# Optimization experiments

Measured on AMD Instinct MI355X. Metric: run time of the kernel, lower is better.

Reference implementation:

```python
import jax, jax.numpy as jnp
import numpy as np

L, H, D, DH, FF, CTX, S, V = 12, 12, 768, 64, 3072, 1536, 8, 1024
B, T = 2, 1024


def setup_inputs() -> dict:
    key = jax.random.key(0)
    ks = jax.random.split(key, 12)
    init = lambda k, shape, fan_in: jax.random.normal(k, shape, jnp.float32) * (fan_in ** -0.5)
    return {
        "prev_tokens": jax.random.randint(ks[0], (B, T, S), 0, V),
        "positions": jnp.tile(jnp.arange(T, dtype=jnp.int32), (B, 1)),
        "intent_vec": jax.random.normal(ks[1], (B, 1, D), jnp.float32) * 0.02,
        "rvq_embed": jax.random.normal(ks[2], (S, V, D), jnp.float32) * 0.02,
        "pos_embed": jax.random.normal(ks[3], (CTX, D), jnp.float32) * 0.02,
        "norm1_w": jnp.ones((L, D), jnp.float32),
        "norm2_w": jnp.ones((L, D), jnp.float32),
        "qkv_w": init(ks[4], (L, 3 * D, D), D),
        "proj_w": init(ks[5], (L, D, D), D),
        "gate_w": init(ks[6], (L, FF, D), D),
        "up_w": init(ks[7], (L, FF, D), D),
        "down_w": init(ks[8], (L, D, FF), FF),
        "normf_w": jnp.ones((D,), jnp.float32),
        "heads_w": init(ks[9], (S, V, D), D),
    }


def _rmsnorm(x, w, eps=1e-6):
    return x * jax.lax.rsqrt(jnp.mean(x * x, axis=-1, keepdims=True) + eps) * w


def reference(prev_tokens, positions, intent_vec, rvq_embed, pos_embed,
              norm1_w, norm2_w, qkv_w, proj_w, gate_w, up_w, down_w,
              normf_w, heads_w):
    # 8-way RVQ embedding sum + positional + intent  -> [B, T, D]
    stage_idx = jnp.arange(S)[None, None, :]               # [1,1,S]
    x = rvq_embed[stage_idx, prev_tokens].sum(axis=2)      # gather [B,T,S,D] -> sum
    x = x + pos_embed[positions] + intent_vec

    scale = DH ** -0.5
    mask = jnp.tril(jnp.ones((T, T), dtype=bool))          # causal (prefill path)

    for l in range(L):
        # attention block (pre-norm)
        h = _rmsnorm(x, norm1_w[l])
        qkv = jnp.einsum('btd,ed->bte', h, qkv_w[l]).reshape(B, T, 3, H, DH)
        q = jnp.moveaxis(qkv[:, :, 0], 1, 2)               # [B,H,T,DH]
        k = jnp.moveaxis(qkv[:, :, 1], 1, 2)
        v = jnp.moveaxis(qkv[:, :, 2], 1, 2)
        att = jnp.einsum('bhqd,bhkd->bhqk', q, k) * scale
        att = jnp.where(mask, att, -jnp.inf)
        att = jax.nn.softmax(att, axis=-1)
        o = jnp.einsum('bhqk,bhkd->bhqd', att, v)
        o = jnp.moveaxis(o, 1, 2).reshape(B, T, D)
        x = x + jnp.einsum('btd,ed->bte', o, proj_w[l])
        # SwiGLU FFN block
        h = _rmsnorm(x, norm2_w[l])
        g = jax.nn.silu(jnp.einsum('btd,fd->btf', h, gate_w[l]))
        u = jnp.einsum('btd,fd->btf', h, up_w[l])
        x = x + jnp.einsum('btf,df->btd', g * u, down_w[l])

    x = _rmsnorm(x, normf_w)
    last = x[:, -1, :]                                     # [B, D]
    logits = jnp.einsum('bd,svd->sbv', last, heads_w)      # per-stage logits [S,B,V]
    return logits
```

## Files before the change

### kernel.cpp

```cpp
#include <hip/hip_runtime.h>
#include <hip/hip_bf16.h>

#define LAYERS 12
#define NH     12
#define D      768
#define DH     64
#define FF     3072
#define NS     8
#define NV     1024
#define BB     2
#define TT     1024
#define BT     (BB*TT)

typedef __attribute__((ext_vector_type(8))) short  short8;
typedef __attribute__((ext_vector_type(8))) unsigned short ushort8;
typedef __attribute__((ext_vector_type(4))) float  floatx4;

__device__ __forceinline__ float wave_sum(float v) {
    v += __shfl_xor(v, 1);  v += __shfl_xor(v, 2);  v += __shfl_xor(v, 4);
    v += __shfl_xor(v, 8);  v += __shfl_xor(v, 16); v += __shfl_xor(v, 32);
    return v;
}
__device__ __forceinline__ unsigned short f2bf(float f) {
    unsigned int u = __builtin_bit_cast(unsigned int, f);
    u += 0x7fffu + ((u >> 16) & 1u);
    return (unsigned short)(u >> 16);
}
__device__ __forceinline__ ushort8 pack8(float4 f0, float4 f1) {
    ushort8 r;
    r[0]=f2bf(f0.x); r[1]=f2bf(f0.y); r[2]=f2bf(f0.z); r[3]=f2bf(f0.w);
    r[4]=f2bf(f1.x); r[5]=f2bf(f1.y); r[6]=f2bf(f1.z); r[7]=f2bf(f1.w);
    return r;
}
__device__ __forceinline__ void gl2lds16(const void* g, void* l) {
    __builtin_amdgcn_global_load_lds(
        (const __attribute__((address_space(1))) unsigned int*)g,
        (__attribute__((address_space(3))) unsigned int*)l, 16, 0, 0);
}

__global__ __launch_bounds__(256) void cvt_bf16_kernel(
    const float* __restrict__ w, unsigned short* __restrict__ o, int n8) {
    const int i = blockIdx.x * 256 + threadIdx.x;
    if (i < n8) {
        const float* p = w + (size_t)i * 8;
        float4 f0 = *(const float4*)p;
        float4 f1 = *(const float4*)(p + 4);
        *(ushort8*)(o + (size_t)i * 8) = pack8(f0, f1);
    }
}

__global__ __launch_bounds__(256) void embed_kernel(
    const int* __restrict__ prev_tokens, const int* __restrict__ positions,
    const float* __restrict__ intent, const float* __restrict__ rvq,
    const float* __restrict__ pos_emb, float* __restrict__ x) {
    const int row = blockIdx.x;
    const int b   = row >> 10;
    __shared__ int toks[NS];
    __shared__ int p;
    if (threadIdx.x < NS) toks[threadIdx.x] = prev_tokens[row * NS + threadIdx.x];
    if (threadIdx.x == NS) p = positions[row];
    __syncthreads();
    for (int d = threadIdx.x; d < D; d += 256) {
        float acc = intent[b * D + d] + pos_emb[p * D + d];
        #pragma unroll
        for (int s = 0; s < NS; ++s)
            acc += rvq[((size_t)(s * NV + toks[s])) * D + d];
        x[(size_t)row * D + d] = acc;
    }
}

__global__ __launch_bounds__(256) void rmsnorm_kernel(
    const float* __restrict__ x, const float* __restrict__ w, unsigned short* __restrict__ h) {
    const int row = blockIdx.x;
    const float* xr = x + (size_t)row * D;
    float ss = 0.f;
    for (int d = threadIdx.x; d < D; d += 256) { float v = xr[d]; ss += v * v; }
    const int wave = threadIdx.x >> 6, lane = threadIdx.x & 63;
    __shared__ float red[4];
    float s = wave_sum(ss);
    if (lane == 0) red[wave] = s;
    __syncthreads();
    float tot = red[0] + red[1] + red[2] + red[3];
    float inv = rsqrtf(tot * (1.0f / D) + 1e-6f);
    for (int d = threadIdx.x; d < D; d += 256)
        h[(size_t)row * D + d] = f2bf(xr[d] * inv * w[d]);
}

template <int MODE, int SPLITK>
__global__ __launch_bounds__(256) void gemm128(
    const unsigned short* __restrict__ A, const unsigned short* __restrict__ W,
    void* __restrict__ Cv, int M, int N, int K) {
    __shared__ unsigned short As[128 * 64];
    __shared__ unsigned short Ws[128 * 64];
    const int tid  = threadIdx.x;
    const int row0 = blockIdx.y * 128;
    const int col0 = blockIdx.x * 128;
    const int kchunk = K / SPLITK;
    const int kbeg = blockIdx.z * kchunk;
    const int kend = kbeg + kchunk;
    const int wv = tid >> 6, lane = tid & 63;
    const int l15 = lane & 15, quad = lane >> 4;
    const int wm = (wv & 1) * 64, wn = (wv >> 1) * 64;
    const int rb = tid >> 3;
    const int sl = tid & 7;

    floatx4 acc[4][4];
    #pragma unroll
    for (int i = 0; i < 4; ++i)
        #pragma unroll
        for (int j = 0; j < 4; ++j) acc[i][j] = (floatx4){0.f, 0.f, 0.f, 0.f};

    for (int k0 = kbeg; k0 < kend; k0 += 64) {
        __syncthreads();
        #pragma unroll
        for (int q = 0; q < 4; ++q) {
            const int r = q * 32 + rb;
            const int gsl = sl ^ (r & 7);
            gl2lds16(A + (size_t)(row0 + r) * K + k0 + gsl * 8,
                     &As[(q * 256 + wv * 64) * 8]);
            gl2lds16(W + (size_t)(col0 + r) * K + k0 + gsl * 8,
                     &Ws[(q * 256 + wv * 64) * 8]);
        }
        __syncthreads();
        #pragma unroll
        for (int ks = 0; ks < 2; ++ks) {
            short8 af[4], bf[4];
            #pragma unroll
            for (int i = 0; i < 4; ++i) {
                const int r = wm + i * 16 + l15;
                af[i] = *(const short8*)(&As[r * 64 + (((ks * 4 + quad) ^ (r & 7)) * 8)]);
            }
            #pragma unroll
            for (int j = 0; j < 4; ++j) {
                const int r = wn + j * 16 + l15;
                bf[j] = *(const short8*)(&Ws[r * 64 + (((ks * 4 + quad) ^ (r & 7)) * 8)]);
            }
            #pragma unroll
            for (int i = 0; i < 4; ++i)
                #pragma unroll
                for (int j = 0; j < 4; ++j)
                    acc[i][j] = __builtin_amdgcn_mfma_f32_16x16x32_bf16(af[i], bf[j], acc[i][j], 0, 0, 0);
        }
    }

    #pragma unroll
    for (int i = 0; i < 4; ++i) {
        #pragma unroll
        for (int j = 0; j < 4; ++j) {
            const int n = col0 + wn + j * 16 + l15;
            #pragma unroll
            for (int r = 0; r < 4; ++r) {
                const int m = row0 + wm + i * 16 + quad * 4 + r;
                const float v = acc[i][j][r];
                if (MODE == 3) {
                    atomicAdd(&((float*)Cv)[(size_t)m * N + n], v);
                } else {
                    const int wsel = n / D;
                    const int rr = n - wsel * D;
                    const int hh = rr >> 6, dd = rr & 63;
                    const int b = m >> 10, t = m & 1023;
                    ((unsigned short*)Cv)[(size_t)wsel * (BT * D) +
                        (((size_t)(b * NH + hh)) * TT + t) * DH + dd] =
                        f2bf(wsel == 0 ? v * 0.125f : v);
                }
            }
        }
    }
}

__global__ __launch_bounds__(256) void gateup128(
    const unsigned short* __restrict__ A, const unsigned short* __restrict__ Wg,
    const unsigned short* __restrict__ Wu, unsigned short* __restrict__ gbf, int K) {
    __shared__ unsigned short As[128 * 64];
    __shared__ unsigned short Gs[64 * 64];
    __shared__ unsigned short Us[64 * 64];
    const int tid  = threadIdx.x;
    const int row0 = blockIdx.y * 128;
    const int col0 = blockIdx.x * 64;
    const int wv = tid >> 6, lane = tid & 63;
    const int l15 = lane & 15, quad = lane >> 4;
    const int wm = (wv & 1) * 64, wn = (wv >> 1) * 32;
    const int rb = tid >> 3;
    const int sl = tid & 7;

    floatx4 ag[4][2], au[4][2];
    #pragma unroll
    for (int i = 0; i < 4; ++i)
        #pragma unroll
        for (int j = 0; j < 2; ++j) {
            ag[i][j] = (floatx4){0.f, 0.f, 0.f, 0.f};
            au[i][j] = (floatx4){0.f, 0.f, 0.f, 0.f};
        }

    for (int k0 = 0; k0 < K; k0 += 64) {
        __syncthreads();
        #pragma unroll
        for (int q = 0; q < 4; ++q) {
            const int r = q * 32 + rb;
            const int gsl = sl ^ (r & 7);
            gl2lds16(A + (size_t)(row0 + r) * K + k0 + gsl * 8,
                     &As[(q * 256 + wv * 64) * 8]);
        }
        {
            #pragma unroll
            for (int q = 0; q < 2; ++q) {
                const int r = q * 32 + rb;
                const int gsl = sl ^ (r & 7);
                gl2lds16(Wg + (size_t)(col0 + r) * K + k0 + gsl * 8,
                         &Gs[(q * 256 + wv * 64) * 8]);
                gl2lds16(Wu + (size_t)(col0 + r) * K + k0 + gsl * 8,
                         &Us[(q * 256 + wv * 64) * 8]);
            }
        }
        __syncthreads();
        #pragma unroll
        for (int ks = 0; ks < 2; ++ks) {
            short8 af[4], bg[2], bu[2];
            #pragma unroll
            for (int i = 0; i < 4; ++i) {
                const int r = wm + i * 16 + l15;
                af[i] = *(const short8*)(&As[r * 64 + (((ks * 4 + quad) ^ (r & 7)) * 8)]);
            }
            #pragma unroll
            for (int j = 0; j < 2; ++j) {
                const int r = wn + j * 16 + l15;
                const int off = r * 64 + (((ks * 4 + quad) ^ (r & 7)) * 8);
                bg[j] = *(const short8*)(&Gs[off]);
                bu[j] = *(const short8*)(&Us[off]);
            }
            #pragma unroll
            for (int i = 0; i < 4; ++i)
                #pragma unroll
                for (int j = 0; j < 2; ++j) {
                    ag[i][j] = __builtin_amdgcn_mfma_f32_16x16x32_bf16(af[i], bg[j], ag[i][j], 0, 0, 0);
                    au[i][j] = __builtin_amdgcn_mfma_f32_16x16x32_bf16(af[i], bu[j], au[i][j], 0, 0, 0);
                }
        }
    }

    #pragma unroll
    for (int i = 0; i < 4; ++i) {
        #pragma unroll
        for (int j = 0; j < 2; ++j) {
            const int n = col0 + wn + j * 16 + l15;
            #pragma unroll
            for (int r = 0; r < 4; ++r) {
                const int m = row0 + wm + i * 16 + quad * 4 + r;
                const float gv = ag[i][j][r], uv = au[i][j][r];
                gbf[(size_t)m * FF + n] = f2bf(gv / (1.f + __expf(-gv)) * uv);
            }
        }
    }
}

#define KP 72
__global__ __launch_bounds__(256) void attn_mfma(
    const unsigned short* __restrict__ qkv, unsigned short* __restrict__ obf) {
    const int bh = blockIdx.y;
    const int b = bh / NH, h = bh - b * NH;
    const int qt = blockIdx.x;
    const int q0 = qt * 64;
    const int tid = threadIdx.x;
    const int wv = tid >> 6, lane = tid & 63;
    const int l15 = lane & 15, quad = lane >> 4;

    const unsigned short* Q = qkv + (size_t)bh * TT * DH;
    const unsigned short* K = qkv + (size_t)BT * D + (size_t)bh * TT * DH;
    const unsigned short* V = qkv + 2 * (size_t)BT * D + (size_t)bh * TT * DH;

    __shared__ unsigned short Ks[64 * KP];
    __shared__ unsigned short Vts[64 * KP];
    __shared__ unsigned short Pa[64 * KP];

    short8 qf[2];
    #pragma unroll
    for (int c = 0; c < 2; ++c)
        qf[c] = *(const short8*)(Q + (size_t)(q0 + wv * 16 + l15) * DH + c * 32 + quad * 8);

    floatx4 o_acc[4];
    #pragma unroll
    for (int j = 0; j < 4; ++j) o_acc[j] = (floatx4){0.f, 0.f, 0.f, 0.f};
    float m_run[4] = {-INFINITY, -INFINITY, -INFINITY, -INFINITY};
    float l_run[4] = {0.f, 0.f, 0.f, 0.f};

    for (int kt = 0; kt <= qt; ++kt) {
        __syncthreads();
        {
            const int krow = tid >> 2, kq = tid & 3;
            const unsigned short* kg = K + (size_t)(kt * 64 + krow) * DH + kq * 16;
            ushort8 k0v = *(const ushort8*)(kg);
            ushort8 k1v = *(const ushort8*)(kg + 8);
            *(ushort8*)(&Ks[krow * KP + kq * 16])     = k0v;
            *(ushort8*)(&Ks[krow * KP + kq * 16 + 8]) = k1v;
            const int kp = tid & 31, chunk = tid >> 5;
            const unsigned short* vg = V + (size_t)(kt * 64 + 2 * kp) * DH + chunk * 8;
            ushort8 v0 = *(const ushort8*)(vg);
            ushort8 v1 = *(const ushort8*)(vg + DH);
            #pragma unroll
            for (int j = 0; j < 8; ++j) {
                unsigned int pk = (unsigned int)v0[j] | ((unsigned int)v1[j] << 16);
                *(unsigned int*)(&Vts[(chunk * 8 + j) * KP + 2 * kp]) = pk;
            }
        }
        __syncthreads();

        floatx4 s[4];
        #pragma unroll
        for (int j = 0; j < 4; ++j) {
            short8 kb0 = *(const short8*)(&Ks[(j * 16 + l15) * KP + quad * 8]);
            short8 kb1 = *(const short8*)(&Ks[(j * 16 + l15) * KP + 32 + quad * 8]);
            floatx4 z = (floatx4){0.f, 0.f, 0.f, 0.f};
            z = __builtin_amdgcn_mfma_f32_16x16x32_bf16(qf[0], kb0, z, 0, 0, 0);
            s[j] = __builtin_amdgcn_mfma_f32_16x16x32_bf16(qf[1], kb1, z, 0, 0, 0);
        }
        if (kt == qt) {
            #pragma unroll
            for (int j = 0; j < 4; ++j) {
                const int k_rel = j * 16 + l15;
                #pragma unroll
                for (int r = 0; r < 4; ++r) {
                    const int q_rel = wv * 16 + quad * 4 + r;
                    if (k_rel > q_rel) s[j][r] = -INFINITY;
                }
            }
        }
        #pragma unroll
        for (int r = 0; r < 4; ++r) {
            float mt = fmaxf(fmaxf(s[0][r], s[1][r]), fmaxf(s[2][r], s[3][r]));
            mt = fmaxf(mt, __shfl_xor(mt, 1));
            mt = fmaxf(mt, __shfl_xor(mt, 2));
            mt = fmaxf(mt, __shfl_xor(mt, 4));
            mt = fmaxf(mt, __shfl_xor(mt, 8));
            const float m_new = fmaxf(m_run[r], mt);
            const float alpha = __expf(m_run[r] - m_new);
            float rs = 0.f;
            #pragma unroll
            for (int j = 0; j < 4; ++j) {
                const float p = __expf(s[j][r] - m_new);
                s[j][r] = p;
                rs += p;
            }
            rs += __shfl_xor(rs, 1);
            rs += __shfl_xor(rs, 2);
            rs += __shfl_xor(rs, 4);
            rs += __shfl_xor(rs, 8);
            l_run[r] = l_run[r] * alpha + rs;
            m_run[r] = m_new;
            #pragma unroll
            for (int j = 0; j < 4; ++j) o_acc[j][r] *= alpha;
        }
        #pragma unroll
        for (int j = 0; j < 4; ++j)
            #pragma unroll
            for (int r = 0; r < 4; ++r)
                Pa[(wv * 16 + quad * 4 + r) * KP + j * 16 + l15] = f2bf(s[j][r]);
        short8 pa0 = *(const short8*)(&Pa[(wv * 16 + l15) * KP + quad * 8]);
        short8 pa1 = *(const short8*)(&Pa[(wv * 16 + l15) * KP + 32 + quad * 8]);
        #pragma unroll
        for (int j = 0; j < 4; ++j) {
            short8 vb0 = *(const short8*)(&Vts[(j * 16 + l15) * KP + quad * 8]);
            short8 vb1 = *(const short8*)(&Vts[(j * 16 + l15) * KP + 32 + quad * 8]);
            o_acc[j] = __builtin_amdgcn_mfma_f32_16x16x32_bf16(pa0, vb0, o_acc[j], 0, 0, 0);
            o_acc[j] = __builtin_amdgcn_mfma_f32_16x16x32_bf16(pa1, vb1, o_acc[j], 0, 0, 0);
        }
    }
    #pragma unroll
    for (int j = 0; j < 4; ++j) {
        #pragma unroll
        for (int r = 0; r < 4; ++r) {
            const int t = q0 + wv * 16 + quad * 4 + r;
            const int ch = h * DH + j * 16 + l15;
            obf[((size_t)(b * TT + t)) * D + ch] = f2bf(o_acc[j][r] / l_run[r]);
        }
    }
}

__global__ __launch_bounds__(256) void final_norm_kernel(
    const float* __restrict__ x, const float* __restrict__ w, float* __restrict__ last) {
    const int b = blockIdx.x;
    const float* xr = x + ((size_t)(b * TT + (TT - 1))) * D;
    float ss = 0.f;
    for (int d = threadIdx.x; d < D; d += 256) { float v = xr[d]; ss += v * v; }
    const int wave = threadIdx.x >> 6, lane = threadIdx.x & 63;
    __shared__ float red[4];
    float s = wave_sum(ss);
    if (lane == 0) red[wave] = s;
    __syncthreads();
    float tot = red[0] + red[1] + red[2] + red[3];
    float inv = rsqrtf(tot * (1.0f / D) + 1e-6f);
    for (int d = threadIdx.x; d < D; d += 256)
        last[(size_t)b * D + d] = xr[d] * inv * w[d];
}

__global__ __launch_bounds__(256) void heads_kernel(
    const float* __restrict__ last, const float* __restrict__ hw, float* __restrict__ out) {
    const int gw = (blockIdx.x * 256 + threadIdx.x) >> 6;
    const int lane = threadIdx.x & 63;
    const int s = gw >> 10, v = gw & 1023;
    const float* w = hw + (size_t)gw * D;
    float a0 = 0.f, a1 = 0.f;
    for (int d = lane; d < D; d += 64) {
        const float ww = w[d];
        a0 = fmaf(ww, last[d], a0);
        a1 = fmaf(ww, last[D + d], a1);
    }
    a0 = wave_sum(a0);
    a1 = wave_sum(a1);
    if (lane == 0) {
        out[((size_t)s * BB + 0) * NV + v] = a0;
        out[((size_t)s * BB + 1) * NV + v] = a1;
    }
}

extern "C" void kernel_launch(void* const* d_in, const int* in_sizes, int n_in,
                              void* d_out, int out_size, void* d_ws, size_t ws_size,
                              hipStream_t stream) {
    const int*   prev_tokens = (const int*)  d_in[0];
    const int*   positions   = (const int*)  d_in[1];
    const float* intent      = (const float*)d_in[2];
    const float* rvq         = (const float*)d_in[3];
    const float* pos_emb     = (const float*)d_in[4];
    const float* norm1_w     = (const float*)d_in[5];
    const float* norm2_w     = (const float*)d_in[6];
    const float* qkv_w       = (const float*)d_in[7];
    const float* proj_w      = (const float*)d_in[8];
    const float* gate_w      = (const float*)d_in[9];
    const float* up_w        = (const float*)d_in[10];
    const float* down_w      = (const float*)d_in[11];
    const float* normf_w     = (const float*)d_in[12];
    const float* heads_w     = (const float*)d_in[13];
    float* out = (float*)d_out;

    char* base = (char*)d_ws;
    float* x   = (float*)base;                       base += (size_t)BT * D * 4;
    float* last= (float*)base;                       base += 4096;
    unsigned short* hbf    = (unsigned short*)base;  base += (size_t)BT * D * 2;
    unsigned short* qkvbf  = (unsigned short*)base;  base += (size_t)3 * BT * D * 2;
    unsigned short* obf    = (unsigned short*)base;  base += (size_t)BT * D * 2;
    unsigned short* gbf    = (unsigned short*)base;  base += (size_t)BT * FF * 2;
    unsigned short* wqkv = (unsigned short*)base;    base += (size_t)LAYERS * 3 * D * D * 2;
    unsigned short* wproj= (unsigned short*)base;    base += (size_t)LAYERS * D * D * 2;
    unsigned short* wgate= (unsigned short*)base;    base += (size_t)LAYERS * FF * D * 2;
    unsigned short* wup  = (unsigned short*)base;    base += (size_t)LAYERS * FF * D * 2;
    unsigned short* wdown= (unsigned short*)base;    base += (size_t)LAYERS * D * FF * 2;

    {
        const int n_qkv  = LAYERS * 3 * D * D / 8;
        const int n_proj = LAYERS * D * D / 8;
        const int n_ff   = LAYERS * FF * D / 8;
        cvt_bf16_kernel<<<(n_qkv  + 255) / 256, 256, 0, stream>>>(qkv_w,  wqkv,  n_qkv);
        cvt_bf16_kernel<<<(n_proj + 255) / 256, 256, 0, stream>>>(proj_w, wproj, n_proj);
        cvt_bf16_kernel<<<(n_ff   + 255) / 256, 256, 0, stream>>>(gate_w, wgate, n_ff);
        cvt_bf16_kernel<<<(n_ff   + 255) / 256, 256, 0, stream>>>(up_w,   wup,   n_ff);
        cvt_bf16_kernel<<<(n_ff   + 255) / 256, 256, 0, stream>>>(down_w, wdown, n_ff);
    }

    embed_kernel<<<BT, 256, 0, stream>>>(prev_tokens, positions, intent, rvq, pos_emb, x);

    for (int l = 0; l < LAYERS; ++l) {
        rmsnorm_kernel<<<BT, 256, 0, stream>>>(x, norm1_w + l * D, hbf);
        gemm128<1, 1><<<dim3(3 * D / 128, BT / 128, 1), 256, 0, stream>>>(
            hbf, wqkv + (size_t)l * 3 * D * D, qkvbf, BT, 3 * D, D);
        attn_mfma<<<dim3(TT / 64, BB * NH), 256, 0, stream>>>(qkvbf, obf);
        gemm128<3, 2><<<dim3(D / 128, BT / 128, 2), 256, 0, stream>>>(
            obf, wproj + (size_t)l * D * D, x, BT, D, D);
        rmsnorm_kernel<<<BT, 256, 0, stream>>>(x, norm2_w + l * D, hbf);
        gateup128<<<dim3(FF / 64, BT / 128), 256, 0, stream>>>(
            hbf, wgate + (size_t)l * FF * D, wup + (size_t)l * FF * D, gbf, D);
        gemm128<3, 4><<<dim3(D / 128, BT / 128, 4), 256, 0, stream>>>(
            gbf, wdown + (size_t)l * D * FF, x, BT, D, FF);
    }

    final_norm_kernel<<<2, 256, 0, stream>>>(x, normf_w, last);
    heads_kernel<<<(NS * NV * 64) / 256, 256, 0, stream>>>(last, heads_w, out);
}
```

Measured before the change: 2.218 ms.

## Enlarge attention key tile and gate-up row tile; wave-per-row rmsnorm

RMSNorm now assigns one wave per row with float4 loads and no shared-memory reduction, launching a quarter of the blocks. The gate/up GEMM tile grows to 256 rows per block, so each wave computes a 64x64 output, doubling weight reuse. Attention processes 128 keys per iteration, with the K tile loaded asynchronously into swizzled LDS and the causal mask applied on absolute indices. These cut loop, sync and bandwidth overhead, but add register pressure in gate/up, halve its block count, and add some masked work in attention.

```diff
diff --git a/kernel.cpp b/kernel.cpp
--- a/kernel.cpp
+++ b/kernel.cpp
@@ -71,19 +71,28 @@
 
 __global__ __launch_bounds__(256) void rmsnorm_kernel(
     const float* __restrict__ x, const float* __restrict__ w, unsigned short* __restrict__ h) {
-    const int row = blockIdx.x;
+    const int row  = blockIdx.x * 4 + (threadIdx.x >> 6);
+    const int lane = threadIdx.x & 63;
     const float* xr = x + (size_t)row * D;
+    float4 v[3];
+    #pragma unroll
+    for (int c = 0; c < 3; ++c) v[c] = *(const float4*)(xr + c * 256 + lane * 4);
     float ss = 0.f;
-    for (int d = threadIdx.x; d < D; d += 256) { float v = xr[d]; ss += v * v; }
-    const int wave = threadIdx.x >> 6, lane = threadIdx.x & 63;
-    __shared__ float red[4];
-    float s = wave_sum(ss);
-    if (lane == 0) red[wave] = s;
-    __syncthreads();
-    float tot = red[0] + red[1] + red[2] + red[3];
-    float inv = rsqrtf(tot * (1.0f / D) + 1e-6f);
-    for (int d = threadIdx.x; d < D; d += 256)
-        h[(size_t)row * D + d] = f2bf(xr[d] * inv * w[d]);
+    #pragma unroll
+    for (int c = 0; c < 3; ++c)
+        ss += v[c].x * v[c].x + v[c].y * v[c].y + v[c].z * v[c].z + v[c].w * v[c].w;
+    ss = wave_sum(ss);
+    const float inv = rsqrtf(ss * (1.0f / D) + 1e-6f);
+    #pragma unroll
+    for (int c = 0; c < 3; ++c) {
+        float4 wv = *(const float4*)(w + c * 256 + lane * 4);
+        ushort4 o;
+        o.x = f2bf(v[c].x * inv * wv.x);
+        o.y = f2bf(v[c].y * inv * wv.y);
+        o.z = f2bf(v[c].z * inv * wv.z);
+        o.w = f2bf(v[c].w * inv * wv.w);
+        *(ushort4*)(h + (size_t)row * D + c * 256 + lane * 4) = o;
+    }
 }
 
 template <int MODE, int SPLITK>
@@ -168,26 +177,26 @@
     }
 }
 
-__global__ __launch_bounds__(256) void gateup128(
+__global__ __launch_bounds__(256) void gateup256(
     const unsigned short* __restrict__ A, const unsigned short* __restrict__ Wg,
     const unsigned short* __restrict__ Wu, unsigned short* __restrict__ gbf, int K) {
-    __shared__ unsigned short As[128 * 64];
+    __shared__ unsigned short As[256 * 64];
     __shared__ unsigned short Gs[64 * 64];
     __shared__ unsigned short Us[64 * 64];
     const int tid  = threadIdx.x;
-    const int row0 = blockIdx.y * 128;
+    const int row0 = blockIdx.y * 256;
     const int col0 = blockIdx.x * 64;
     const int wv = tid >> 6, lane = tid & 63;
     const int l15 = lane & 15, quad = lane >> 4;
-    const int wm = (wv & 1) * 64, wn = (wv >> 1) * 32;
+    const int wm = wv * 64;
     const int rb = tid >> 3;
     const int sl = tid & 7;
 
-    floatx4 ag[4][2], au[4][2];
+    floatx4 ag[4][4], au[4][4];
     #pragma unroll
     for (int i = 0; i < 4; ++i)
         #pragma unroll
-        for (int j = 0; j < 2; ++j) {
+        for (int j = 0; j < 4; ++j) {
             ag[i][j] = (floatx4){0.f, 0.f, 0.f, 0.f};
             au[i][j] = (floatx4){0.f, 0.f, 0.f, 0.f};
         }
@@ -195,35 +204,33 @@
     for (int k0 = 0; k0 < K; k0 += 64) {
         __syncthreads();
         #pragma unroll
-        for (int q = 0; q < 4; ++q) {
+        for (int q = 0; q < 8; ++q) {
             const int r = q * 32 + rb;
             const int gsl = sl ^ (r & 7);
             gl2lds16(A + (size_t)(row0 + r) * K + k0 + gsl * 8,
                      &As[(q * 256 + wv * 64) * 8]);
         }
-        {
-            #pragma unroll
-            for (int q = 0; q < 2; ++q) {
-                const int r = q * 32 + rb;
-                const int gsl = sl ^ (r & 7);
-                gl2lds16(Wg + (size_t)(col0 + r) * K + k0 + gsl * 8,
-                         &Gs[(q * 256 + wv * 64) * 8]);
-                gl2lds16(Wu + (size_t)(col0 + r) * K + k0 + gsl * 8,
-                         &Us[(q * 256 + wv * 64) * 8]);
-            }
+        #pragma unroll
+        for (int q = 0; q < 2; ++q) {
+            const int r = q * 32 + rb;
+            const int gsl = sl ^ (r & 7);
+            gl2lds16(Wg + (size_t)(col0 + r) * K + k0 + gsl * 8,
+                     &Gs[(q * 256 + wv * 64) * 8]);
+            gl2lds16(Wu + (size_t)(col0 + r) * K + k0 + gsl * 8,
+                     &Us[(q * 256 + wv * 64) * 8]);
         }
         __syncthreads();
         #pragma unroll
         for (int ks = 0; ks < 2; ++ks) {
-            short8 af[4], bg[2], bu[2];
+            short8 af[4], bg[4], bu[4];
             #pragma unroll
             for (int i = 0; i < 4; ++i) {
                 const int r = wm + i * 16 + l15;
                 af[i] = *(const short8*)(&As[r * 64 + (((ks * 4 + quad) ^ (r & 7)) * 8)]);
             }
             #pragma unroll
-            for (int j = 0; j < 2; ++j) {
-                const int r = wn + j * 16 + l15;
+            for (int j = 0; j < 4; ++j) {
+                const int r = j * 16 + l15;
                 const int off = r * 64 + (((ks * 4 + quad) ^ (r & 7)) * 8);
                 bg[j] = *(const short8*)(&Gs[off]);
                 bu[j] = *(const short8*)(&Us[off]);
@@ -231,7 +238,7 @@
             #pragma unroll
             for (int i = 0; i < 4; ++i)
                 #pragma unroll
-                for (int j = 0; j < 2; ++j) {
+                for (int j = 0; j < 4; ++j) {
                     ag[i][j] = __builtin_amdgcn_mfma_f32_16x16x32_bf16(af[i], bg[j], ag[i][j], 0, 0, 0);
                     au[i][j] = __builtin_amdgcn_mfma_f32_16x16x32_bf16(af[i], bu[j], au[i][j], 0, 0, 0);
                 }
@@ -241,8 +248,8 @@
     #pragma unroll
     for (int i = 0; i < 4; ++i) {
         #pragma unroll
-        for (int j = 0; j < 2; ++j) {
-            const int n = col0 + wn + j * 16 + l15;
+        for (int j = 0; j < 4; ++j) {
+            const int n = col0 + j * 16 + l15;
             #pragma unroll
             for (int r = 0; r < 4; ++r) {
                 const int m = row0 + wm + i * 16 + quad * 4 + r;
@@ -253,7 +260,7 @@
     }
 }
 
-#define KP 72
+#define KP2 136
 __global__ __launch_bounds__(256) void attn_mfma(
     const unsigned short* __restrict__ qkv, unsigned short* __restrict__ obf) {
     const int bh = blockIdx.y;
@@ -268,9 +275,9 @@
     const unsigned short* K = qkv + (size_t)BT * D + (size_t)bh * TT * DH;
     const unsigned short* V = qkv + 2 * (size_t)BT * D + (size_t)bh * TT * DH;
 
-    __shared__ unsigned short Ks[64 * KP];
-    __shared__ unsigned short Vts[64 * KP];
-    __shared__ unsigned short Pa[64 * KP];
+    __shared__ unsigned short Ks[128 * 64];
+    __shared__ unsigned short Vts[64 * KP2];
+    __shared__ unsigned short Pa[64 * KP2];
 
     short8 qf[2];
     #pragma unroll
@@ -283,50 +290,61 @@
     float m_run[4] = {-INFINITY, -INFINITY, -INFINITY, -INFINITY};
     float l_run[4] = {0.f, 0.f, 0.f, 0.f};
 
-    for (int kt = 0; kt <= qt; ++kt) {
-        __syncthreads();
+    const int rb = tid >> 3, sl = tid & 7;
+    const int nkt = (q0 >> 7) + 1;
+    for (int kt = 0; kt < nkt; ++kt) {
+        const int k0 = kt * 128;
+        __syncthreads();
+        #pragma unroll
+        for (int q = 0; q < 4; ++q) {
+            const int r = q * 32 + rb;
+            const int gsl = sl ^ (r & 7);
+            gl2lds16(K + (size_t)(k0 + r) * DH + gsl * 8,
+                     &Ks[(q * 256 + wv * 64) * 8]);
+        }
         {
-            const int krow = tid >> 2, kq = tid & 3;
-            const unsigned short* kg = K + (size_t)(kt * 64 + krow) * DH + kq * 16;
-            ushort8 k0v = *(const ushort8*)(kg);
-            ushort8 k1v = *(const ushort8*)(kg + 8);
-            *(ushort8*)(&Ks[krow * KP + kq * 16])     = k0v;
-            *(ushort8*)(&Ks[krow * KP + kq * 16 + 8]) = k1v;
             const int kp = tid & 31, chunk = tid >> 5;
-            const unsigned short* vg = V + (size_t)(kt * 64 + 2 * kp) * DH + chunk * 8;
-            ushort8 v0 = *(const ushort8*)(vg);
-            ushort8 v1 = *(const ushort8*)(vg + DH);
-            #pragma unroll
-            for (int j = 0; j < 8; ++j) {
-                unsigned int pk = (unsigned int)v0[j] | ((unsigned int)v1[j] << 16);
-                *(unsigned int*)(&Vts[(chunk * 8 + j) * KP + 2 * kp]) = pk;
-            }
-        }
-        __syncthreads();
-
-        floatx4 s[4];
-        #pragma unroll
-        for (int j = 0; j < 4; ++j) {
-            short8 kb0 = *(const short8*)(&Ks[(j * 16 + l15) * KP + quad * 8]);
-            short8 kb1 = *(const short8*)(&Ks[(j * 16 + l15) * KP + 32 + quad * 8]);
+            #pragma unroll
+            for (int half = 0; half < 2; ++half) {
+                const int kk = half * 64 + 2 * kp;
+                const unsigned short* vg = V + (size_t)(k0 + kk) * DH + chunk * 8;
+                ushort8 v0 = *(const ushort8*)(vg);
+                ushort8 v1 = *(const ushort8*)(vg + DH);
+                #pragma unroll
+                for (int j = 0; j < 8; ++j) {
+                    unsigned int pk = (unsigned int)v0[j] | ((unsigned int)v1[j] << 16);
+                    *(unsigned int*)(&Vts[(chunk * 8 + j) * KP2 + kk]) = pk;
+                }
+            }
+        }
+        __syncthreads();
+
+        floatx4 s[8];
+        #pragma unroll
+        for (int j = 0; j < 8; ++j) {
+            const int r = j * 16 + l15;
+            short8 kb0 = *(const short8*)(&Ks[r * 64 + ((quad ^ (r & 7)) * 8)]);
+            short8 kb1 = *(const short8*)(&Ks[r * 64 + (((4 + quad) ^ (r & 7)) * 8)]);
             floatx4 z = (floatx4){0.f, 0.f, 0.f, 0.f};
             z = __builtin_amdgcn_mfma_f32_16x16x32_bf16(qf[0], kb0, z, 0, 0, 0);
             s[j] = __builtin_amdgcn_mfma_f32_16x16x32_bf16(qf[1], kb1, z, 0, 0, 0);
         }
-        if (kt == qt) {
-            #pragma unroll
-            for (int j = 0; j < 4; ++j) {
-                const int k_rel = j * 16 + l15;
+        if (kt == nkt - 1) {
+            #pragma unroll
+            for (int j = 0; j < 8; ++j) {
+                const int k_abs = k0 + j * 16 + l15;
                 #pragma unroll
                 for (int r = 0; r < 4; ++r) {
-                    const int q_rel = wv * 16 + quad * 4 + r;
-                    if (k_rel > q_rel) s[j][r] = -INFINITY;
+                    const int q_abs = q0 + wv * 16 + quad * 4 + r;
+                    if (k_abs > q_abs) s[j][r] = -INFINITY;
                 }
             }
         }
         #pragma unroll
         for (int r = 0; r < 4; ++r) {
-            float mt = fmaxf(fmaxf(s[0][r], s[1][r]), fmaxf(s[2][r], s[3][r]));
+            float mt = s[0][r];
+            #pragma unroll
+            for (int j = 1; j < 8; ++j) mt = fmaxf(mt, s[j][r]);
             mt = fmaxf(mt, __shfl_xor(mt, 1));
             mt = fmaxf(mt, __shfl_xor(mt, 2));
             mt = fmaxf(mt, __shfl_xor(mt, 4));
@@ -335,7 +353,7 @@
             const float alpha = __expf(m_run[r] - m_new);
             float rs = 0.f;
             #pragma unroll
-            for (int j = 0; j < 4; ++j) {
+            for (int j = 0; j < 8; ++j) {
                 const float p = __expf(s[j][r] - m_new);
                 s[j][r] = p;
                 rs += p;
@@ -347,21 +365,24 @@
             l_run[r] = l_run[r] * alpha + rs;
             m_run[r] = m_new;
             #pragma unroll
-            for (int j = 0; j < 4; ++j) o_acc[j][r] *= alpha;
-        }
-        #pragma unroll
-        for (int j = 0; j < 4; ++j)
+            for (int jo = 0; jo < 4; ++jo) o_acc[jo][r] *= alpha;
+        }
+        #pragma unroll
+        for (int j = 0; j < 8; ++j)
             #pragma unroll
             for (int r = 0; r < 4; ++r)
-                Pa[(wv * 16 + quad * 4 + r) * KP + j * 16 + l15] = f2bf(s[j][r]);
-        short8 pa0 = *(const short8*)(&Pa[(wv * 16 + l15) * KP + quad * 8]);
-        short8 pa1 = *(const short8*)(&Pa[(wv * 16 + l15) * KP + 32 + quad * 8]);
+                Pa[(wv * 16 + quad * 4 + r) * KP2 + j * 16 + l15] = f2bf(s[j][r]);
+        short8 pa[4];
+        #pragma unroll
+        for (int c = 0; c < 4; ++c)
+            pa[c] = *(const short8*)(&Pa[(wv * 16 + l15) * KP2 + c * 32 + quad * 8]);
         #pragma unroll
         for (int j = 0; j < 4; ++j) {
-            short8 vb0 = *(const short8*)(&Vts[(j * 16 + l15) * KP + quad * 8]);
-            short8 vb1 = *(const short8*)(&Vts[(j * 16 + l15) * KP + 32 + quad * 8]);
-            o_acc[j] = __builtin_amdgcn_mfma_f32_16x16x32_bf16(pa0, vb0, o_acc[j], 0, 0, 0);
-            o_acc[j] = __builtin_amdgcn_mfma_f32_16x16x32_bf16(pa1, vb1, o_acc[j], 0, 0, 0);
+            #pragma unroll
+            for (int c = 0; c < 4; ++c) {
+                short8 vb = *(const short8*)(&Vts[(j * 16 + l15) * KP2 + c * 32 + quad * 8]);
+                o_acc[j] = __builtin_amdgcn_mfma_f32_16x16x32_bf16(pa[c], vb, o_acc[j], 0, 0, 0);
+            }
         }
     }
     #pragma unroll
@@ -458,14 +479,14 @@
     embed_kernel<<<BT, 256, 0, stream>>>(prev_tokens, positions, intent, rvq, pos_emb, x);
 
     for (int l = 0; l < LAYERS; ++l) {
-        rmsnorm_kernel<<<BT, 256, 0, stream>>>(x, norm1_w + l * D, hbf);
+        rmsnorm_kernel<<<BT / 4, 256, 0, stream>>>(x, norm1_w + l * D, hbf);
         gemm128<1, 1><<<dim3(3 * D / 128, BT / 128, 1), 256, 0, stream>>>(
             hbf, wqkv + (size_t)l * 3 * D * D, qkvbf, BT, 3 * D, D);
         attn_mfma<<<dim3(TT / 64, BB * NH), 256, 0, stream>>>(qkvbf, obf);
         gemm128<3, 2><<<dim3(D / 128, BT / 128, 2), 256, 0, stream>>>(
             obf, wproj + (size_t)l * D * D, x, BT, D, D);
-        rmsnorm_kernel<<<BT, 256, 0, stream>>>(x, norm2_w + l * D, hbf);
-        gateup128<<<dim3(FF / 64, BT / 128), 256, 0, stream>>>(
+        rmsnorm_kernel<<<BT / 4, 256, 0, stream>>>(x, norm2_w + l * D, hbf);
+        gateup256<<<dim3(FF / 64, BT / 256), 256, 0, stream>>>(
             hbf, wgate + (size_t)l * FF * D, wup + (size_t)l * FF * D, gbf, D);
         gemm128<3, 4><<<dim3(D / 128, BT / 128, 4), 256, 0, stream>>>(
             gbf, wdown + (size_t)l * D * FF, x, BT, D, FF);
```

Measured after the change: 2.443 ms. 10.1% more time.
